# Optimization experiments

Measured on AMD Instinct MI355X. Metric: run time of the kernel, lower is better.

Reference implementation:

```python
import jax, jax.numpy as jnp
import numpy as np

B, L, D_MODEL = 2, 1024, 1024
N_LAYERS = 2
D_INNER = 2 * D_MODEL          # expand = 2
D_STATE = 16
D_CONV = 4
DT_RANK = (D_MODEL + 15) // 16  # ceil(d_model/16) = 64
INIT_SCALE = 0.02


def setup_inputs() -> dict:
    key = jax.random.key(0)
    ks = jax.random.split(key, 8)
    f32 = jnp.float32
    dt_init = float(np.log(np.expm1(0.01)))  # softplus^-1(0.01), standard mamba dt bias init
    return {
        "x": jax.random.normal(ks[0], (B, L, D_MODEL), f32),
        "W_in": jax.random.normal(ks[1], (N_LAYERS, 2 * D_INNER, D_MODEL), f32) * INIT_SCALE,
        "conv_w": jax.random.normal(ks[2], (N_LAYERS, D_INNER, D_CONV), f32) * INIT_SCALE,
        "conv_b": jnp.zeros((N_LAYERS, D_INNER), f32),
        "W_x": jax.random.normal(ks[3], (N_LAYERS, DT_RANK + 2 * D_STATE, D_INNER), f32) * INIT_SCALE,
        "W_dt": jax.random.normal(ks[4], (N_LAYERS, D_INNER, DT_RANK), f32) * INIT_SCALE,
        "b_dt": jnp.full((N_LAYERS, D_INNER), dt_init, f32),
        "A_log": jnp.tile(jnp.log(jnp.arange(1, D_STATE + 1, dtype=f32)), (N_LAYERS, D_INNER, 1)),
        "D": jnp.ones((N_LAYERS, D_INNER), f32),
        "W_out": jax.random.normal(ks[5], (N_LAYERS, D_MODEL, D_INNER), f32) * INIT_SCALE,
    }


def _silu(x):
    return x * jax.nn.sigmoid(x)


def _causal_conv1d(u, w, b):
    # u: [B, L, D_INNER], w: [D_INNER, D_CONV] depthwise, b: [D_INNER]
    ut = jnp.pad(jnp.transpose(u, (0, 2, 1)), ((0, 0), (0, 0), (D_CONV - 1, 0)))
    y = jax.lax.conv_general_dilated(
        ut, w[:, None, :], window_strides=(1,), padding='VALID',
        feature_group_count=D_INNER, dimension_numbers=('NCH', 'OIH', 'NCH'))
    return jnp.transpose(y + b[None, :, None], (0, 2, 1))


def _selective_scan(u, dt, A, Bm, Cm, Dvec):
    # u, dt: [B, L, D_INNER]; A: [D_INNER, N]; Bm, Cm: [B, L, N]; Dvec: [D_INNER]
    dA = jnp.exp(dt[..., None] * A)                        # [B,L,Din,N]
    dBu = dt[..., None] * Bm[:, :, None, :] * u[..., None]  # [B,L,Din,N]

    def step(h, xs):
        dA_t, dBu_t, C_t = xs                              # [B,Din,N],[B,Din,N],[B,N]
        h = dA_t * h + dBu_t
        y = jnp.einsum('bdn,bn->bd', h, C_t)
        return h, y

    h0 = jnp.zeros((u.shape[0], D_INNER, D_STATE), u.dtype)
    _, ys = jax.lax.scan(step, h0, (jnp.swapaxes(dA, 0, 1),
                                    jnp.swapaxes(dBu, 0, 1),
                                    jnp.swapaxes(Cm, 0, 1)))
    return jnp.swapaxes(ys, 0, 1) + u * Dvec               # [B,L,Din]


def _mamba_layer(x, W_in, conv_w, conv_b, W_x, W_dt, b_dt, A_log, Dvec, W_out):
    xz = jnp.einsum('bld,ed->ble', x, W_in)                # [B,L,2*Din]
    u, z = jnp.split(xz, 2, axis=-1)
    u = _silu(_causal_conv1d(u, conv_w, conv_b))
    x_dbl = jnp.einsum('bld,rd->blr', u, W_x)              # [B,L,dt_rank+2N]
    dt, Bm, Cm = jnp.split(x_dbl, [DT_RANK, DT_RANK + D_STATE], axis=-1)
    dt = jax.nn.softplus(jnp.einsum('blr,dr->bld', dt, W_dt) + b_dt)
    A = -jnp.exp(A_log)
    y = _selective_scan(u, dt, A, Bm, Cm, Dvec)
    y = y * _silu(z)
    return jnp.einsum('bld,od->blo', y, W_out)


def reference(x, W_in, conv_w, conv_b, W_x, W_dt, b_dt, A_log, D, W_out):
    residual = x
    h = x
    for i in range(N_LAYERS):
        h = _mamba_layer(h, W_in[i], conv_w[i], conv_b[i], W_x[i],
                         W_dt[i], b_dt[i], A_log[i], D[i], W_out[i])
    return h + residual
```

## Files before the change

kernel.cpp:

```cpp
#include <hip/hip_runtime.h>
#include <hip/hip_bf16.h>
#include <math.h>

#define B_ 2
#define L_ 1024
#define DM 1024
#define DIN 2048
#define DS 16
#define DTR 64
#define CHL 32
#define NCH 32

typedef __attribute__((ext_vector_type(8))) short bf16x8;
typedef __attribute__((ext_vector_type(8))) unsigned short u16x8;
typedef __attribute__((ext_vector_type(4))) unsigned short u16x4;
typedef __attribute__((ext_vector_type(4))) float f32x4;
typedef unsigned short ushort_t;
typedef unsigned int uint_t;

__device__ __forceinline__ float sigmoidf_(float x) { return 1.f / (1.f + __expf(-x)); }
__device__ __forceinline__ ushort_t f2b(float f) {
    uint_t b = __float_as_uint(f);
    return (ushort_t)((b + 0x7FFFu + ((b >> 16) & 1u)) >> 16);
}
__device__ __forceinline__ float b2f(ushort_t u) {
    return __uint_as_float(((uint_t)u) << 16);
}

__global__ __launch_bounds__(256) void f2b_all_k(
    const float* __restrict__ s0, ushort_t* __restrict__ d0, int n0,
    const float* __restrict__ s1, ushort_t* __restrict__ d1, int n1,
    const float* __restrict__ s2, ushort_t* __restrict__ d2, int n2,
    const float* __restrict__ s3, ushort_t* __restrict__ d3, int n3,
    const float* __restrict__ s4, ushort_t* __restrict__ d4, int n4)
{
    int i = (blockIdx.x * 256 + threadIdx.x) * 4;
    const float* s; ushort_t* d;
    if (i < n0) { s = s0; d = d0; }
    else { i -= n0;
    if (i < n1) { s = s1; d = d1; }
    else { i -= n1;
    if (i < n2) { s = s2; d = d2; }
    else { i -= n2;
    if (i < n3) { s = s3; d = d3; }
    else { i -= n3;
    if (i < n4) { s = s4; d = d4; }
    else return; }}}}
    float4 v = *(const float4*)(s + i);
    u16x4 o;
    o[0] = f2b(v.x); o[1] = f2b(v.y); o[2] = f2b(v.z); o[3] = f2b(v.w);
    *(u16x4*)(d + i) = o;
}

__device__ __forceinline__ int xcd_swz(int wgid, int nwg) {
    int cpx = nwg >> 3;
    return (wgid & 7) * cpx + (wgid >> 3);
}

__global__ __launch_bounds__(256) void mgemm_in(const ushort_t* __restrict__ A,
    const ushort_t* __restrict__ Bt, ushort_t* __restrict__ Cb,
    int M, int N, int K, int lda, int ldb)
{
    __shared__ ushort_t sA[2][128 * 32];
    __shared__ ushort_t sB[2][128 * 32];
    const int tid = threadIdx.x;
    const int lane = tid & 63, wv = tid >> 6;
    const int wm = wv >> 1, wn = wv & 1;
    const int swz = xcd_swz(blockIdx.y * gridDim.x + blockIdx.x, gridDim.x * gridDim.y);
    const int m0 = (swz / gridDim.x) * 128, n0 = (swz % gridDim.x) * 128;
    const int sr = tid >> 2;
    const int sc = (tid & 3) * 8;
    f32x4 acc[4][4] = {};

#pragma unroll
    for (int j = 0; j < 2; ++j) {
        int ra = sr + j * 64;
        __builtin_amdgcn_global_load_lds(
            (const uint_t*)(A + (size_t)(m0 + ra) * lda + sc),
            (uint_t*)(sA[0] + ra * 32 + sc), 16, 0, 0);
        __builtin_amdgcn_global_load_lds(
            (const uint_t*)(Bt + (size_t)(n0 + ra) * ldb + sc),
            (uint_t*)(sB[0] + ra * 32 + sc), 16, 0, 0);
    }
    __syncthreads();
    int cur = 0;
    for (int k0 = 0; k0 < K; k0 += 32) {
        if (k0 + 32 < K) {
            int nxt = cur ^ 1;
#pragma unroll
            for (int j = 0; j < 2; ++j) {
                int ra = sr + j * 64;
                __builtin_amdgcn_global_load_lds(
                    (const uint_t*)(A + (size_t)(m0 + ra) * lda + k0 + 32 + sc),
                    (uint_t*)(sA[nxt] + ra * 32 + sc), 16, 0, 0);
                __builtin_amdgcn_global_load_lds(
                    (const uint_t*)(Bt + (size_t)(n0 + ra) * ldb + k0 + 32 + sc),
                    (uint_t*)(sB[nxt] + ra * 32 + sc), 16, 0, 0);
            }
        }
        bf16x8 af[4], bfr[4];
#pragma unroll
        for (int i = 0; i < 4; ++i) {
            af[i]  = *(const bf16x8*)(sA[cur] + (wm * 64 + i * 16 + (lane & 15)) * 32 + (lane >> 4) * 8);
            bfr[i] = *(const bf16x8*)(sB[cur] + (wn * 64 + i * 16 + (lane & 15)) * 32 + (lane >> 4) * 8);
        }
#pragma unroll
        for (int i = 0; i < 4; ++i)
#pragma unroll
            for (int jj = 0; jj < 4; ++jj)
                acc[i][jj] = __builtin_amdgcn_mfma_f32_16x16x32_bf16(af[i], bfr[jj], acc[i][jj], 0, 0, 0);
        __syncthreads();
        cur ^= 1;
    }

    const int cr = (lane >> 4) * 4, cc = lane & 15;
#pragma unroll
    for (int i = 0; i < 4; ++i) {
        int mrow = m0 + wm * 64 + i * 16 + cr;
#pragma unroll
        for (int jj = 0; jj < 4; ++jj) {
            int ncol = n0 + wn * 64 + jj * 16 + cc;
#pragma unroll
            for (int r = 0; r < 4; ++r)
                Cb[(size_t)(mrow + r) * N + ncol] = f2b(acc[i][jj][r]);
        }
    }
}

__global__ __launch_bounds__(256) void mgemm_sk(const ushort_t* __restrict__ A,
    const ushort_t* __restrict__ Bt, float* __restrict__ P,
    int M, int N, int Kslice, int lda, int ldb)
{
    __shared__ ushort_t sA[2][128 * 32];
    __shared__ ushort_t sB[2][128 * 32];
    const int tid = threadIdx.x;
    const int lane = tid & 63, wv = tid >> 6;
    const int wm = wv >> 1, wn = wv & 1;
    const int m0 = blockIdx.y * 128;
    const int kbase = blockIdx.z * Kslice;
    const int sr = tid >> 2;
    const int sc = (tid & 3) * 8;
    f32x4 acc[4][4] = {};

#pragma unroll
    for (int j = 0; j < 2; ++j) {
        int ra = sr + j * 64;
        __builtin_amdgcn_global_load_lds(
            (const uint_t*)(A + (size_t)(m0 + ra) * lda + kbase + sc),
            (uint_t*)(sA[0] + ra * 32 + sc), 16, 0, 0);
        int gb = ra; if (gb >= N) gb = N - 1;
        __builtin_amdgcn_global_load_lds(
            (const uint_t*)(Bt + (size_t)gb * ldb + kbase + sc),
            (uint_t*)(sB[0] + ra * 32 + sc), 16, 0, 0);
    }
    __syncthreads();
    int cur = 0;
    for (int k0 = kbase; k0 < kbase + Kslice; k0 += 32) {
        if (k0 + 32 < kbase + Kslice) {
            int nxt = cur ^ 1;
#pragma unroll
            for (int j = 0; j < 2; ++j) {
                int ra = sr + j * 64;
                __builtin_amdgcn_global_load_lds(
                    (const uint_t*)(A + (size_t)(m0 + ra) * lda + k0 + 32 + sc),
                    (uint_t*)(sA[nxt] + ra * 32 + sc), 16, 0, 0);
                int gb = ra; if (gb >= N) gb = N - 1;
                __builtin_amdgcn_global_load_lds(
                    (const uint_t*)(Bt + (size_t)gb * ldb + k0 + 32 + sc),
                    (uint_t*)(sB[nxt] + ra * 32 + sc), 16, 0, 0);
            }
        }
        bf16x8 af[4], bfr[4];
#pragma unroll
        for (int i = 0; i < 4; ++i) {
            af[i]  = *(const bf16x8*)(sA[cur] + (wm * 64 + i * 16 + (lane & 15)) * 32 + (lane >> 4) * 8);
            bfr[i] = *(const bf16x8*)(sB[cur] + (wn * 64 + i * 16 + (lane & 15)) * 32 + (lane >> 4) * 8);
        }
#pragma unroll
        for (int i = 0; i < 4; ++i)
#pragma unroll
            for (int jj = 0; jj < 4; ++jj)
                acc[i][jj] = __builtin_amdgcn_mfma_f32_16x16x32_bf16(af[i], bfr[jj], acc[i][jj], 0, 0, 0);
        __syncthreads();
        cur ^= 1;
    }

    const int cr = (lane >> 4) * 4, cc = lane & 15;
    float* Pz = P + (size_t)blockIdx.z * M * 96;
#pragma unroll
    for (int i = 0; i < 4; ++i) {
        int mrow = m0 + wm * 64 + i * 16 + cr;
#pragma unroll
        for (int jj = 0; jj < 4; ++jj) {
            int ncol = wn * 64 + jj * 16 + cc;
            if (ncol < 96) {
#pragma unroll
                for (int r = 0; r < 4; ++r)
                    Pz[(size_t)(mrow + r) * 96 + ncol] = acc[i][jj][r];
            }
        }
    }
}

__global__ __launch_bounds__(256) void mgemm_dtf(const float* __restrict__ P,
    const ushort_t* __restrict__ Wd, const float* __restrict__ bias,
    float* __restrict__ xdbl, ushort_t* __restrict__ dtfb)
{
    __shared__ ushort_t sA[2][128 * 36];
    __shared__ ushort_t sB[2][128 * 32];
    const int tid = threadIdx.x;
    const int lane = tid & 63, wv = tid >> 6;
    const int wm = wv >> 1, wn = wv & 1;
    const int n0 = blockIdx.x * 128, m0 = blockIdx.y * 128;

#pragma unroll
    for (int kh = 0; kh < 2; ++kh)
#pragma unroll
        for (int it = 0; it < 2; ++it) {
            int ci = tid + it * 256;
            int row = ci >> 2, cc = ci & 3;
            __builtin_amdgcn_global_load_lds(
                (const uint_t*)(Wd + (size_t)(n0 + row) * 64 + kh * 32 + cc * 8),
                (uint_t*)(sB[kh] + (size_t)ci * 8), 16, 0, 0);
        }

#pragma unroll
    for (int it = 0; it < 8; ++it) {
        int ci = tid + it * 256;
        int row = ci >> 4, c4 = (ci & 15) * 4;
        float s0 = 0.f, s1 = 0.f, s2 = 0.f, s3 = 0.f;
#pragma unroll
        for (int z = 0; z < 8; ++z) {
            f32x4 v = *(const f32x4*)(P + (size_t)z * 196608 + (size_t)(m0 + row) * 96 + c4);
            s0 += v[0]; s1 += v[1]; s2 += v[2]; s3 += v[3];
        }
        u16x4 o; o[0] = f2b(s0); o[1] = f2b(s1); o[2] = f2b(s2); o[3] = f2b(s3);
        int kh = c4 >> 5, cl = c4 & 31;
        *(u16x4*)(sA[kh] + row * 36 + cl) = o;
    }
    if (blockIdx.x == 0) {
#pragma unroll
        for (int it = 0; it < 4; ++it) {
            int ci = tid + it * 256;
            int row = ci >> 3, c4 = (ci & 7) * 4;
            f32x4 s = {0.f, 0.f, 0.f, 0.f};
#pragma unroll
            for (int z = 0; z < 8; ++z) {
                f32x4 v = *(const f32x4*)(P + (size_t)z * 196608 + (size_t)(m0 + row) * 96 + 64 + c4);
                s[0] += v[0]; s[1] += v[1]; s[2] += v[2]; s[3] += v[3];
            }
            *(f32x4*)(xdbl + (size_t)(m0 + row) * 96 + 64 + c4) = s;
        }
    }
    __syncthreads();

    f32x4 acc[4][4] = {};
#pragma unroll
    for (int ks = 0; ks < 2; ++ks) {
        bf16x8 af[4], bfr[4];
#pragma unroll
        for (int i = 0; i < 4; ++i) {
            af[i]  = *(const bf16x8*)(sA[ks] + (wm * 64 + i * 16 + (lane & 15)) * 36 + (lane >> 4) * 8);
            bfr[i] = *(const bf16x8*)(sB[ks] + (wn * 64 + i * 16 + (lane & 15)) * 32 + (lane >> 4) * 8);
        }
#pragma unroll
        for (int i = 0; i < 4; ++i)
#pragma unroll
            for (int jj = 0; jj < 4; ++jj)
                acc[i][jj] = __builtin_amdgcn_mfma_f32_16x16x32_bf16(af[i], bfr[jj], acc[i][jj], 0, 0, 0);
    }

    const int cr = (lane >> 4) * 4, cc = lane & 15;
#pragma unroll
    for (int i = 0; i < 4; ++i) {
        int mrow = m0 + wm * 64 + i * 16 + cr;
#pragma unroll
        for (int jj = 0; jj < 4; ++jj) {
            int ncol = n0 + wn * 64 + jj * 16 + cc;
#pragma unroll
            for (int r = 0; r < 4; ++r) {
                float s = acc[i][jj][r] + bias[ncol];
                dtfb[(size_t)(mrow + r) * DIN + ncol] =
                    f2b((s > 20.f) ? s : log1pf(expf(s)));
            }
        }
    }
}

__global__ __launch_bounds__(256) void mgemm_o(const ushort_t* __restrict__ A,
    const ushort_t* __restrict__ Bt, float* __restrict__ P,
    int M, int N, int Kslice, int lda, int ldb)
{
    __shared__ ushort_t sA[2][128 * 32];
    __shared__ ushort_t sB[2][64 * 32];
    const int tid = threadIdx.x;
    const int lane = tid & 63, wv = tid >> 6;
    const int m0 = blockIdx.y * 128, n0 = blockIdx.x * 64;
    const int kbase = blockIdx.z * Kslice;
    const int sr = tid >> 2;
    const int sc = (tid & 3) * 8;
    f32x4 acc[2][4] = {};

#pragma unroll
    for (int j = 0; j < 2; ++j) {
        int ra = sr + j * 64;
        __builtin_amdgcn_global_load_lds(
            (const uint_t*)(A + (size_t)(m0 + ra) * lda + kbase + sc),
            (uint_t*)(sA[0] + ra * 32 + sc), 16, 0, 0);
    }
    __builtin_amdgcn_global_load_lds(
        (const uint_t*)(Bt + (size_t)(n0 + sr) * ldb + kbase + sc),
        (uint_t*)(sB[0] + sr * 32 + sc), 16, 0, 0);
    __syncthreads();
    int cur = 0;
    for (int k0 = kbase; k0 < kbase + Kslice; k0 += 32) {
        if (k0 + 32 < kbase + Kslice) {
            int nxt = cur ^ 1;
#pragma unroll
            for (int j = 0; j < 2; ++j) {
                int ra = sr + j * 64;
                __builtin_amdgcn_global_load_lds(
                    (const uint_t*)(A + (size_t)(m0 + ra) * lda + k0 + 32 + sc),
                    (uint_t*)(sA[nxt] + ra * 32 + sc), 16, 0, 0);
            }
            __builtin_amdgcn_global_load_lds(
                (const uint_t*)(Bt + (size_t)(n0 + sr) * ldb + k0 + 32 + sc),
                (uint_t*)(sB[nxt] + sr * 32 + sc), 16, 0, 0);
        }
        bf16x8 af[2], bfr[4];
#pragma unroll
        for (int i = 0; i < 2; ++i)
            af[i]  = *(const bf16x8*)(sA[cur] + (wv * 32 + i * 16 + (lane & 15)) * 32 + (lane >> 4) * 8);
#pragma unroll
        for (int jj = 0; jj < 4; ++jj)
            bfr[jj] = *(const bf16x8*)(sB[cur] + (jj * 16 + (lane & 15)) * 32 + (lane >> 4) * 8);
#pragma unroll
        for (int i = 0; i < 2; ++i)
#pragma unroll
            for (int jj = 0; jj < 4; ++jj)
                acc[i][jj] = __builtin_amdgcn_mfma_f32_16x16x32_bf16(af[i], bfr[jj], acc[i][jj], 0, 0, 0);
        __syncthreads();
        cur ^= 1;
    }

    const int cr = (lane >> 4) * 4, cc = lane & 15;
    float* Pz = P + (size_t)blockIdx.z * M * DM;
#pragma unroll
    for (int i = 0; i < 2; ++i) {
        int mrow = m0 + wv * 32 + i * 16 + cr;
#pragma unroll
        for (int jj = 0; jj < 4; ++jj) {
            int ncol = n0 + jj * 16 + cc;
#pragma unroll
            for (int r = 0; r < 4; ++r)
                Pz[(size_t)(mrow + r) * DM + ncol] = acc[i][jj][r];
        }
    }
}

template<int EPI>
__global__ __launch_bounds__(256) void ored_k(const float* __restrict__ P,
    const float* __restrict__ res, float* __restrict__ Cf, ushort_t* __restrict__ Cb)
{
    int i = (blockIdx.x * 256 + threadIdx.x) * 4;
    f32x4 a = *(const f32x4*)(P + i);
    f32x4 b = *(const f32x4*)(P + 2097152 + i);
    if (EPI == 3) {
        u16x4 o;
#pragma unroll
        for (int e = 0; e < 4; ++e) o[e] = f2b(a[e] + b[e]);
        *(u16x4*)(Cb + i) = o;
    } else {
        f32x4 r = *(const f32x4*)(res + i);
        f32x4 o;
#pragma unroll
        for (int e = 0; e < 4; ++e) o[e] = a[e] + b[e] + r[e];
        *(f32x4*)(Cf + i) = o;
    }
}

__global__ __launch_bounds__(256) void conv8_k(const ushort_t* __restrict__ xzb,
    const float* __restrict__ cw, const float* __restrict__ cb,
    ushort_t* __restrict__ ucb)
{
    int idx8 = blockIdx.x * 256 + threadIdx.x;
    int d8 = (idx8 & 255) * 8;
    int t = (idx8 >> 8) & (L_ - 1);
    int b = idx8 >> 18;
    const ushort_t* base = xzb + (size_t)b * L_ * (2 * DIN) + d8;
    float acc[8];
    const float4* cb4 = (const float4*)(cb + d8);
    float4 cbl = cb4[0], cbh = cb4[1];
#pragma unroll
    for (int e = 0; e < 4; ++e) { acc[e] = ((const float*)&cbl)[e]; acc[4 + e] = ((const float*)&cbh)[e]; }
    float4 cwv[8];
#pragma unroll
    for (int e = 0; e < 8; ++e) cwv[e] = ((const float4*)cw)[d8 + e];
#pragma unroll
    for (int j = 0; j < 4; ++j) {
        int tt = t - 3 + j;
        if (tt >= 0) {
            u16x8 row = *(const u16x8*)(base + (size_t)tt * (2 * DIN));
#pragma unroll
            for (int e = 0; e < 8; ++e)
                acc[e] = fmaf(((const float*)&cwv[e])[j], b2f(row[e]), acc[e]);
        }
    }
    u16x8 ob;
#pragma unroll
    for (int e = 0; e < 8; ++e) {
        float v = acc[e] * sigmoidf_(acc[e]);
        ob[e] = f2b(v);
    }
    *(u16x8*)(ucb + (size_t)idx8 * 8) = ob;
}

__global__ __launch_bounds__(256, 2) void scan_s1(const ushort_t* __restrict__ dtfb,
    const ushort_t* __restrict__ ucb, const float* __restrict__ xdbl,
    const float* __restrict__ A_log,
    float* __restrict__ bnd_q, float* __restrict__ bnd_s)
{
    __shared__ ushort_t s_dt[CHL * 256];
    __shared__ ushort_t s_u[CHL * 256];
    __shared__ float sB[CHL * 16];
    const int tid = threadIdx.x;
    const int bx = blockIdx.x;
    const int dg = bx & 7, c = (bx >> 3) & 31, b = bx >> 8;
    const int d = dg * 256 + tid;
    const int dbase = dg * 256;
    const int row0 = b * L_ + c * CHL;

    float A_dn[16];
#pragma unroll
    for (int n = 0; n < 16; ++n) A_dn[n] = -__expf(A_log[(size_t)d * DS + n]);

    const int rr = tid >> 5, c16 = (tid & 31) * 8;
#pragma unroll
    for (int it = 0; it < 4; ++it) {
        int k = rr + it * 8;
        size_t gro = (size_t)(row0 + k) * DIN + dbase + c16;
        __builtin_amdgcn_global_load_lds((const uint_t*)(dtfb + gro),
            (uint_t*)(s_dt + k * 256 + c16), 16, 0, 0);
        __builtin_amdgcn_global_load_lds((const uint_t*)(ucb + gro),
            (uint_t*)(s_u + k * 256 + c16), 16, 0, 0);
    }
#pragma unroll
    for (int j = 0; j < 2; ++j) {
        int idx = tid + j * 256;
        int t = idx >> 4, n = idx & 15;
        sB[idx] = xdbl[(size_t)(row0 + t) * 96 + 64 + n];
    }
    __syncthreads();

    float q[16];
#pragma unroll
    for (int n = 0; n < 16; ++n) q[n] = 0.f;
    float s = 0.f;
    for (int k = 0; k < CHL; ++k) {
        float dtv = b2f(s_dt[k * 256 + tid]);
        float uv  = b2f(s_u[k * 256 + tid]);
        float dtu = dtv * uv;
        s += dtv;
        f32x4 Bq[4];
#pragma unroll
        for (int j = 0; j < 4; ++j) Bq[j] = *(const f32x4*)(sB + k * 16 + j * 4);
#pragma unroll
        for (int n = 0; n < 16; ++n)
            q[n] = fmaf(__expf(dtv * A_dn[n]), q[n], dtu * Bq[n >> 2][n & 3]);
    }
    float* qp = bnd_q + ((size_t)(b * NCH + c) * DIN + d) * 16;
#pragma unroll
    for (int j = 0; j < 4; ++j)
        *(f32x4*)(qp + j * 4) = (f32x4){q[j * 4], q[j * 4 + 1], q[j * 4 + 2], q[j * 4 + 3]};
    bnd_s[(size_t)(b * NCH + c) * DIN + d] = s;
}

__global__ __launch_bounds__(256, 2) void scan_s2(const ushort_t* __restrict__ dtfb,
    const ushort_t* __restrict__ ucb_in, const float* __restrict__ xdbl,
    const ushort_t* __restrict__ xzb, const float* __restrict__ A_log,
    const float* __restrict__ Dvec, const float* __restrict__ bnd_q,
    const float* __restrict__ bnd_s, ushort_t* __restrict__ ucb_out)
{
    __shared__ ushort_t s_dt[CHL * 256];
    __shared__ ushort_t s_u[CHL * 256];
    __shared__ ushort_t s_z[CHL * 256];
    __shared__ float sBC[CHL * 32];
    const int tid = threadIdx.x;
    const int bx = blockIdx.x;
    const int dg = bx & 7, c = (bx >> 3) & 31, b = bx >> 8;
    const int d = dg * 256 + tid;
    const int dbase = dg * 256;
    const int row0 = b * L_ + c * CHL;
    const float Dd = Dvec[d];

    float A_dn[16];
#pragma unroll
    for (int n = 0; n < 16; ++n) A_dn[n] = -__expf(A_log[(size_t)d * DS + n]);

    const int rr = tid >> 5, c16 = (tid & 31) * 8;
#pragma unroll
    for (int it = 0; it < 4; ++it) {
        int k = rr + it * 8;
        size_t gro = (size_t)(row0 + k) * DIN + dbase + c16;
        __builtin_amdgcn_global_load_lds((const uint_t*)(dtfb + gro),
            (uint_t*)(s_dt + k * 256 + c16), 16, 0, 0);
        __builtin_amdgcn_global_load_lds((const uint_t*)(ucb_in + gro),
            (uint_t*)(s_u + k * 256 + c16), 16, 0, 0);
        __builtin_amdgcn_global_load_lds(
            (const uint_t*)(xzb + (size_t)(row0 + k) * (2 * DIN) + DIN + dbase + c16),
            (uint_t*)(s_z + k * 256 + c16), 16, 0, 0);
    }
#pragma unroll
    for (int j = 0; j < 4; ++j) {
        int idx = tid + j * 256;
        int t = idx >> 5, jj = idx & 31;
        sBC[idx] = xdbl[(size_t)(row0 + t) * 96 + 64 + (jj & 1) * 16 + (jj >> 1)];
    }

    float h[16];
#pragma unroll
    for (int n = 0; n < 16; ++n) h[n] = 0.f;
    const size_t cb_base = (size_t)b * NCH * DIN + d;
    for (int cc = 0; cc < c; ++cc) {
        size_t idx = cb_base + (size_t)cc * DIN;
        float sv = bnd_s[idx];
        const float* qp = bnd_q + idx * 16;
        f32x4 qv[4];
#pragma unroll
        for (int j = 0; j < 4; ++j) qv[j] = *(const f32x4*)(qp + j * 4);
#pragma unroll
        for (int n = 0; n < 16; ++n)
            h[n] = fmaf(__expf(A_dn[n] * sv), h[n], qv[n >> 2][n & 3]);
    }
    __syncthreads();

    for (int k = 0; k < CHL; ++k) {
        float dtv = b2f(s_dt[k * 256 + tid]);
        float uv  = b2f(s_u[k * 256 + tid]);
        float z   = b2f(s_z[k * 256 + tid]);
        float dtu = dtv * uv;
        float y = uv * Dd;
        f32x4 bcq[8];
#pragma unroll
        for (int j = 0; j < 8; ++j) bcq[j] = *(const f32x4*)(sBC + k * 32 + j * 4);
#pragma unroll
        for (int n = 0; n < 16; ++n) {
            float Bv = bcq[n >> 1][(n & 1) * 2];
            float Cv = bcq[n >> 1][(n & 1) * 2 + 1];
            h[n] = fmaf(__expf(dtv * A_dn[n]), h[n], dtu * Bv);
            y = fmaf(h[n], Cv, y);
        }
        y *= z * sigmoidf_(z);
        s_dt[k * 256 + tid] = f2b(y);
    }
    __syncthreads();
#pragma unroll
    for (int it = 0; it < 4; ++it) {
        int k = rr + it * 8;
        *(u16x8*)(ucb_out + (size_t)(row0 + k) * DIN + dbase + c16) =
            *(const u16x8*)(s_dt + k * 256 + c16);
    }
}

extern "C" void kernel_launch(void* const* d_in, const int* in_sizes, int n_in,
                              void* d_out, int out_size, void* d_ws, size_t ws_size,
                              hipStream_t stream)
{
    (void)in_sizes; (void)n_in; (void)out_size; (void)ws_size;
    const float* x      = (const float*)d_in[0];
    const float* W_in   = (const float*)d_in[1];
    const float* conv_w = (const float*)d_in[2];
    const float* conv_b = (const float*)d_in[3];
    const float* W_x    = (const float*)d_in[4];
    const float* W_dt   = (const float*)d_in[5];
    const float* b_dt   = (const float*)d_in[6];
    const float* A_log  = (const float*)d_in[7];
    const float* Dv     = (const float*)d_in[8];
    const float* W_out  = (const float*)d_in[9];
    float* out = (float*)d_out;

    float* xdbl    = (float*)d_ws;
    float* pws     = xdbl + 196608;
    float* bnd_q   = pws + 1572864;
    float* bnd_s   = bnd_q + 2097152;
    ushort_t* dtfb = (ushort_t*)(bnd_s + 131072);
    ushort_t* xzb  = dtfb + 4194304;
    ushort_t* ucb  = xzb + 8388608;
    ushort_t* xb   = ucb + 4194304;
    ushort_t* wib  = xb + 2097152;
    ushort_t* wxb  = wib + 8388608;
    ushort_t* wdb  = wxb + 393216;
    ushort_t* wob  = wdb + 262144;
    float* pwo     = (float*)(wob + 4194304);

    const int M = B_ * L_;
    const int NT = 2097152 + 8388608 + 393216 + 262144 + 4194304;
    f2b_all_k<<<(NT / 4) / 256, 256, 0, stream>>>(
        x, xb, 2097152, W_in, wib, 8388608, W_x, wxb, 393216,
        W_dt, wdb, 262144, W_out, wob, 4194304);

    for (int layer = 0; layer < 2; ++layer) {
        mgemm_in<<<dim3(4096 / 128, M / 128), 256, 0, stream>>>(
            xb, wib + (size_t)layer * 4194304, xzb, M, 2 * DIN, DM, DM, DM);
        conv8_k<<<(B_ * L_ * DIN / 8) / 256, 256, 0, stream>>>(
            xzb, conv_w + (size_t)layer * DIN * 4, conv_b + (size_t)layer * DIN, ucb);
        mgemm_sk<<<dim3(1, M / 128, 8), 256, 0, stream>>>(
            ucb, wxb + (size_t)layer * 196608, pws, M, 96, DIN / 8, DIN, DIN);
        mgemm_dtf<<<dim3(16, 16), 256, 0, stream>>>(
            pws, wdb + (size_t)layer * 131072, b_dt + (size_t)layer * DIN, xdbl, dtfb);
        const float* Al = A_log + (size_t)layer * DIN * DS;
        scan_s1<<<B_ * NCH * 8, 256, 0, stream>>>(dtfb, ucb, xdbl, Al, bnd_q, bnd_s);
        scan_s2<<<B_ * NCH * 8, 256, 0, stream>>>(dtfb, ucb, xdbl, xzb, Al,
            Dv + (size_t)layer * DIN, bnd_q, bnd_s, ucb);
        mgemm_o<<<dim3(1024 / 64, M / 128, 2), 256, 0, stream>>>(
            ucb, wob + (size_t)layer * 2097152, pwo, M, DM, DIN / 2, DIN, DIN);
        if (layer == 0)
            ored_k<3><<<(2097152 / 4) / 256, 256, 0, stream>>>(pwo, nullptr, nullptr, xb);
        else
            ored_k<4><<<(2097152 / 4) / 256, 256, 0, stream>>>(pwo, x, out, nullptr);
    }
}
```

Before: 436.5 us.

## Add separate chunk-boundary prefix scan kernel and halve scan chunk length

Before, each scan_s2 block rebuilt its starting state by folding all earlier chunk summaries, which is quadratic redundant work over the chunks. A new scan_b2 kernel now runs the inter-chunk recurrence once per (batch, channel, state) and writes the carried-in state back in place, so scan_s2 only loads its initial h. Chunk length drops from 32 to 16, which doubles block count and parallelism for the two intra-chunk passes. A_log loads are vectorized, and the boundary buffers are aliased onto the dead pws and pwo workspace regions. The trade-off is an extra launch and a sequential 64-step dependent loop in scan_b2.

```diff
diff --git a/kernel.cpp b/kernel.cpp
--- a/kernel.cpp
+++ b/kernel.cpp
@@ -8,8 +8,8 @@
 #define DIN 2048
 #define DS 16
 #define DTR 64
-#define CHL 32
-#define NCH 32
+#define CHL 16
+#define NCH 64
 
 typedef __attribute__((ext_vector_type(8))) short bf16x8;
 typedef __attribute__((ext_vector_type(8))) unsigned short u16x8;
@@ -425,18 +425,22 @@
     __shared__ float sB[CHL * 16];
     const int tid = threadIdx.x;
     const int bx = blockIdx.x;
-    const int dg = bx & 7, c = (bx >> 3) & 31, b = bx >> 8;
+    const int dg = bx & 7, c = (bx >> 3) & (NCH - 1), b = bx >> 9;
     const int d = dg * 256 + tid;
     const int dbase = dg * 256;
     const int row0 = b * L_ + c * CHL;
 
     float A_dn[16];
 #pragma unroll
-    for (int n = 0; n < 16; ++n) A_dn[n] = -__expf(A_log[(size_t)d * DS + n]);
+    for (int j = 0; j < 4; ++j) {
+        f32x4 av = *(const f32x4*)(A_log + (size_t)d * DS + j * 4);
+#pragma unroll
+        for (int e = 0; e < 4; ++e) A_dn[j * 4 + e] = -__expf(av[e]);
+    }
 
     const int rr = tid >> 5, c16 = (tid & 31) * 8;
 #pragma unroll
-    for (int it = 0; it < 4; ++it) {
+    for (int it = 0; it < 2; ++it) {
         int k = rr + it * 8;
         size_t gro = (size_t)(row0 + k) * DIN + dbase + c16;
         __builtin_amdgcn_global_load_lds((const uint_t*)(dtfb + gro),
@@ -444,12 +448,7 @@
         __builtin_amdgcn_global_load_lds((const uint_t*)(ucb + gro),
             (uint_t*)(s_u + k * 256 + c16), 16, 0, 0);
     }
-#pragma unroll
-    for (int j = 0; j < 2; ++j) {
-        int idx = tid + j * 256;
-        int t = idx >> 4, n = idx & 15;
-        sB[idx] = xdbl[(size_t)(row0 + t) * 96 + 64 + n];
-    }
+    sB[tid] = xdbl[(size_t)(row0 + (tid >> 4)) * 96 + 64 + (tid & 15)];
     __syncthreads();
 
     float q[16];
@@ -475,11 +474,27 @@
     bnd_s[(size_t)(b * NCH + c) * DIN + d] = s;
 }
 
+__global__ __launch_bounds__(256) void scan_b2(float* __restrict__ bnd_q,
+    const float* __restrict__ bnd_s, const float* __restrict__ A_log)
+{
+    int glob = blockIdx.x * 256 + threadIdx.x;
+    int n = glob & 15, d = (glob >> 4) & (DIN - 1), b = glob >> 15;
+    float A_dn = -__expf(A_log[(size_t)d * DS + n]);
+    float H = 0.f;
+    for (int c = 0; c < NCH; ++c) {
+        size_t idx = (size_t)(b * NCH + c) * DIN + d;
+        float q = bnd_q[idx * 16 + n];
+        float sv = bnd_s[idx];
+        bnd_q[idx * 16 + n] = H;
+        H = fmaf(__expf(A_dn * sv), H, q);
+    }
+}
+
 __global__ __launch_bounds__(256, 2) void scan_s2(const ushort_t* __restrict__ dtfb,
     const ushort_t* __restrict__ ucb_in, const float* __restrict__ xdbl,
     const ushort_t* __restrict__ xzb, const float* __restrict__ A_log,
     const float* __restrict__ Dvec, const float* __restrict__ bnd_q,
-    const float* __restrict__ bnd_s, ushort_t* __restrict__ ucb_out)
+    ushort_t* __restrict__ ucb_out)
 {
     __shared__ ushort_t s_dt[CHL * 256];
     __shared__ ushort_t s_u[CHL * 256];
@@ -487,7 +502,7 @@
     __shared__ float sBC[CHL * 32];
     const int tid = threadIdx.x;
     const int bx = blockIdx.x;
-    const int dg = bx & 7, c = (bx >> 3) & 31, b = bx >> 8;
+    const int dg = bx & 7, c = (bx >> 3) & (NCH - 1), b = bx >> 9;
     const int d = dg * 256 + tid;
     const int dbase = dg * 256;
     const int row0 = b * L_ + c * CHL;
@@ -495,11 +510,15 @@
 
     float A_dn[16];
 #pragma unroll
-    for (int n = 0; n < 16; ++n) A_dn[n] = -__expf(A_log[(size_t)d * DS + n]);
+    for (int j = 0; j < 4; ++j) {
+        f32x4 av = *(const f32x4*)(A_log + (size_t)d * DS + j * 4);
+#pragma unroll
+        for (int e = 0; e < 4; ++e) A_dn[j * 4 + e] = -__expf(av[e]);
+    }
 
     const int rr = tid >> 5, c16 = (tid & 31) * 8;
 #pragma unroll
-    for (int it = 0; it < 4; ++it) {
+    for (int it = 0; it < 2; ++it) {
         int k = rr + it * 8;
         size_t gro = (size_t)(row0 + k) * DIN + dbase + c16;
         __builtin_amdgcn_global_load_lds((const uint_t*)(dtfb + gro),
@@ -511,26 +530,19 @@
             (uint_t*)(s_z + k * 256 + c16), 16, 0, 0);
     }
 #pragma unroll
-    for (int j = 0; j < 4; ++j) {
+    for (int j = 0; j < 2; ++j) {
         int idx = tid + j * 256;
         int t = idx >> 5, jj = idx & 31;
         sBC[idx] = xdbl[(size_t)(row0 + t) * 96 + 64 + (jj & 1) * 16 + (jj >> 1)];
     }
 
     float h[16];
-#pragma unroll
-    for (int n = 0; n < 16; ++n) h[n] = 0.f;
-    const size_t cb_base = (size_t)b * NCH * DIN + d;
-    for (int cc = 0; cc < c; ++cc) {
-        size_t idx = cb_base + (size_t)cc * DIN;
-        float sv = bnd_s[idx];
-        const float* qp = bnd_q + idx * 16;
-        f32x4 qv[4];
-#pragma unroll
-        for (int j = 0; j < 4; ++j) qv[j] = *(const f32x4*)(qp + j * 4);
-#pragma unroll
-        for (int n = 0; n < 16; ++n)
-            h[n] = fmaf(__expf(A_dn[n] * sv), h[n], qv[n >> 2][n & 3]);
+    const float* hp = bnd_q + ((size_t)(b * NCH + c) * DIN + d) * 16;
+#pragma unroll
+    for (int j = 0; j < 4; ++j) {
+        f32x4 hv = *(const f32x4*)(hp + j * 4);
+#pragma unroll
+        for (int e = 0; e < 4; ++e) h[j * 4 + e] = hv[e];
     }
     __syncthreads();
 
@@ -555,7 +567,7 @@
     }
     __syncthreads();
 #pragma unroll
-    for (int it = 0; it < 4; ++it) {
+    for (int it = 0; it < 2; ++it) {
         int k = rr + it * 8;
         *(u16x8*)(ucb_out + (size_t)(row0 + k) * DIN + dbase + c16) =
             *(const u16x8*)(s_dt + k * 256 + c16);
@@ -581,9 +593,8 @@
 
     float* xdbl    = (float*)d_ws;
     float* pws     = xdbl + 196608;
-    float* bnd_q   = pws + 1572864;
-    float* bnd_s   = bnd_q + 2097152;
-    ushort_t* dtfb = (ushort_t*)(bnd_s + 131072);
+    float* bnd_s   = pws;
+    ushort_t* dtfb = (ushort_t*)(pws + 1572864);
     ushort_t* xzb  = dtfb + 4194304;
     ushort_t* ucb  = xzb + 8388608;
     ushort_t* xb   = ucb + 4194304;
@@ -592,6 +603,7 @@
     ushort_t* wdb  = wxb + 393216;
     ushort_t* wob  = wdb + 262144;
     float* pwo     = (float*)(wob + 4194304);
+    float* bnd_q   = pwo;
 
     const int M = B_ * L_;
     const int NT = 2097152 + 8388608 + 393216 + 262144 + 4194304;
@@ -610,8 +622,9 @@
             pws, wdb + (size_t)layer * 131072, b_dt + (size_t)layer * DIN, xdbl, dtfb);
         const float* Al = A_log + (size_t)layer * DIN * DS;
         scan_s1<<<B_ * NCH * 8, 256, 0, stream>>>(dtfb, ucb, xdbl, Al, bnd_q, bnd_s);
+        scan_b2<<<(B_ * DIN * 16) / 256, 256, 0, stream>>>(bnd_q, bnd_s, Al);
         scan_s2<<<B_ * NCH * 8, 256, 0, stream>>>(dtfb, ucb, xdbl, xzb, Al,
-            Dv + (size_t)layer * DIN, bnd_q, bnd_s, ucb);
+            Dv + (size_t)layer * DIN, bnd_q, ucb);
         mgemm_o<<<dim3(1024 / 64, M / 128, 2), 256, 0, stream>>>(
             ucb, wob + (size_t)layer * 2097152, pwo, M, DM, DIN / 2, DIN, DIN);
         if (layer == 0)
```

Measured after the change: 425.6 us. -2.5%, faster.
